# Kernel tuning notes

Hardware: AMD Instinct MI355X
Metric: run time of the kernel (lower is better)

The kernel has to match this reference:

```python
import jax, jax.numpy as jnp
import numpy as np

B, T, I, H, O = 128, 500, 512, 1024, 11
BETA, THRESH, GAMMA, SPARSITY = 0.9, 1.0, 0.5, 0.05

@jax.custom_vjp
def spike(x):
    return (x > 0).astype(x.dtype)

def _spike_fwd(x):
    return (x > 0).astype(x.dtype), x

def _spike_bwd(x, g):
    # surrogate gradient: gamma / (1 + |x|)^2
    return (g * GAMMA / jnp.square(1.0 + jnp.abs(x)),)

spike.defvjp(_spike_fwd, _spike_bwd)


def setup_inputs() -> dict:
    key = jax.random.key(0)
    k0, k1, k2, k3, k4 = jax.random.split(key, 5)
    x = jax.random.normal(k0, (B, T, I), jnp.float32)
    # xavier-uniform-like init for W_in / W_out, orthogonal-ish (scaled normal) for W_rec
    lim_in = (6.0 / (I + H)) ** 0.5
    lim_out = (6.0 / (H + O)) ** 0.5
    W_in = jax.random.uniform(k1, (I, H), jnp.float32, -lim_in, lim_in)
    W_rec = jax.random.normal(k2, (H, H), jnp.float32) / jnp.sqrt(jnp.float32(H))
    W_out = jax.random.uniform(k3, (H, O), jnp.float32, -lim_out, lim_out)
    # fixed sparse connectivity mask: Bernoulli(sparsity), no self-connections
    mask = (jax.random.uniform(k4, (H, H)) < SPARSITY).astype(jnp.float32)
    mask = mask * (1.0 - jnp.eye(H, dtype=jnp.float32))
    W_rec = W_rec * mask  # reset_parameters() applies mask at init when mask is not learnable
    h_bias = jnp.zeros((H,), jnp.float32)
    b_out = jnp.zeros((O,), jnp.float32)
    return {"x": x, "W_in": W_in, "W_rec": W_rec, "W_out": W_out,
            "h_bias": h_bias, "b_out": b_out, "mask": mask}


def reference(x, W_in, W_rec, W_out, h_bias, b_out, mask):
    W_eff = W_rec * mask                                   # masked recurrent weights [H,H]
    drive = jnp.einsum('bti,ih->bth', x, W_in) + h_bias    # per-step input drive [B,T,H]
    drive_t = jnp.swapaxes(drive, 0, 1)                    # [T,B,H]

    def step(carry, d_t):
        v, s = carry
        v = BETA * v + d_t + s @ W_eff                     # LIF membrane update
        s_new = spike(v - THRESH)                          # surrogate threshold spike
        v = v - jax.lax.stop_gradient(s_new) * THRESH      # subtract reset (detached)
        out_t = s_new @ W_out + b_out                      # per-step readout [B,O]
        return (v, s_new), out_t

    init = (jnp.zeros((x.shape[0], W_eff.shape[0]), x.dtype),
            jnp.zeros((x.shape[0], W_eff.shape[0]), x.dtype))
    _, outs = jax.lax.scan(step, init, drive_t)            # outs: [T,B,O]
    return jnp.mean(outs, axis=0)                          # 'rate' readout -> [B,O]
```

## Files before the change

kernel.cpp:

```cpp
#include <hip/hip_runtime.h>
#include <cstdint>
#include <cstddef>

#define B_ 128
#define T_ 500
#define I_ 512
#define H_ 1024
#define O_ 11
#define BETA 0.9f
#define THRESH 1.0f
#define K2_ 1536

typedef __attribute__((ext_vector_type(4))) float f32x4;
typedef __attribute__((ext_vector_type(8))) short bf16x8;
typedef __attribute__((ext_vector_type(4))) unsigned int u32x4;

__device__ __forceinline__ unsigned short bf16_rne(float f) {
  unsigned int u = __float_as_uint(f);
  unsigned int r = u + 0x7FFFu + ((u >> 16) & 1u);
  return (unsigned short)(r >> 16);
}
__device__ __forceinline__ float bf16_to_f(unsigned short h) {
  return __uint_as_float(((unsigned int)h) << 16);
}

__global__ void k_csr(const float* __restrict__ W_rec, const float* __restrict__ mask,
                      unsigned int* __restrict__ csr, unsigned int* __restrict__ rowhi) {
  int r = blockIdx.x * 4 + (threadIdx.x >> 6);
  int lane = threadIdx.x & 63;
  unsigned cnt = 0;
  const float* mrow = mask + (size_t)r * H_;
  const float* wrow = W_rec + (size_t)r * H_;
  for (int c = 0; c < 16; ++c) {
    float m = mrow[c * 64 + lane];
    bool nz = (m != 0.f);
    unsigned long long bb = __ballot(nz);
    unsigned pos = cnt + (unsigned)__popcll(bb & ((1ull << lane) - 1ull));
    if (nz) {
      float w = wrow[c * 64 + lane] * m;
      int wi = __float2int_rn(w * 8388608.f);
      wi = wi > 2097151 ? 2097151 : (wi < -2097151 ? -2097151 : wi);
      if (pos < 128u) csr[((size_t)r << 7) + pos] = (((unsigned)wi) << 10) | (unsigned)(c * 64 + lane);
    }
    cnt += (unsigned)__popcll(bb);
  }
  for (unsigned p = (cnt > 128u ? 128u : cnt) + (unsigned)lane; p < 128u; p += 64u)
    csr[((size_t)r << 7) + p] = (p & 63u);
  if (lane == 0) rowhi[r] = (cnt > 64u) ? 1u : 0u;
}

__global__ void k_build_wt(const float* __restrict__ W_in, unsigned short* __restrict__ Wt) {
  int n = blockIdx.y;
  int k2 = blockIdx.x * 256 + threadIdx.x;
  int i = k2 & 511;
  int c = k2 >> 9;
  float w = W_in[i * H_ + n];
  unsigned short hi = bf16_rne(w);
  unsigned short v = (c == 2) ? bf16_rne(w - bf16_to_f(hi)) : hi;
  Wt[(size_t)n * K2_ + k2] = v;
}

#define LDA 72
__global__ __launch_bounds__(512, 1) void k_gemm(const float* __restrict__ x,
                                                 const unsigned short* __restrict__ Wt,
                                                 float* __restrict__ drive,
                                                 int t0, int Tc) {
  __shared__ __align__(16) unsigned short As[128 * LDA];
  __shared__ __align__(16) unsigned short Bs[256 * LDA];
  int id = blockIdx.x;
  int mt = (id >> 5) * 8 + (id & 7);
  int nt = (id >> 3) & 3;
  if (mt >= Tc) return;
  int tid = threadIdx.x;
  int lane = tid & 63, w = tid >> 6;
  int wr = w >> 2, wc = w & 3;
  f32x4 acc[4][4] = {};
  int arow = tid >> 2, aq = tid & 3;
  int brow = tid >> 1, bh = tid & 1;
  int rr = mt * 128 + arow;
  int bb = rr / Tc, tt = rr - bb * Tc;
  const float* xrow = x + ((size_t)(bb * T_ + t0 + tt)) * I_ + aq * 16;
  const unsigned short* wtrow = Wt + (size_t)(nt * 256 + brow) * K2_ + bh * 32;
  for (int kt = 0; kt < K2_ / 64; ++kt) {
    int creg = kt >> 3;
    int i0 = (kt & 7) * 64;
    const float* ap = xrow + i0;
    float4 a0 = *(const float4*)(ap);
    float4 a1 = *(const float4*)(ap + 4);
    float4 a2 = *(const float4*)(ap + 8);
    float4 a3 = *(const float4*)(ap + 12);
    u32x4 b0 = *(const u32x4*)(wtrow + kt * 64);
    u32x4 b1 = *(const u32x4*)(wtrow + kt * 64 + 8);
    u32x4 b2 = *(const u32x4*)(wtrow + kt * 64 + 16);
    u32x4 b3 = *(const u32x4*)(wtrow + kt * 64 + 24);
    alignas(16) unsigned short o[16];
    float vv[16] = {a0.x, a0.y, a0.z, a0.w, a1.x, a1.y, a1.z, a1.w,
                    a2.x, a2.y, a2.z, a2.w, a3.x, a3.y, a3.z, a3.w};
#pragma unroll
    for (int j = 0; j < 16; ++j) {
      unsigned short hi = bf16_rne(vv[j]);
      o[j] = (creg == 1) ? bf16_rne(vv[j] - bf16_to_f(hi)) : hi;
    }
    __syncthreads();
    *(u32x4*)&As[arow * LDA + aq * 16] = *(u32x4*)o;
    *(u32x4*)&As[arow * LDA + aq * 16 + 8] = *(u32x4*)(o + 8);
    *(u32x4*)&Bs[brow * LDA + bh * 32] = b0;
    *(u32x4*)&Bs[brow * LDA + bh * 32 + 8] = b1;
    *(u32x4*)&Bs[brow * LDA + bh * 32 + 16] = b2;
    *(u32x4*)&Bs[brow * LDA + bh * 32 + 24] = b3;
    __syncthreads();
#pragma unroll
    for (int kk = 0; kk < 2; ++kk) {
      bf16x8 af[4], bf[4];
#pragma unroll
      for (int mi = 0; mi < 4; ++mi)
        af[mi] = *(const bf16x8*)&As[(wr * 64 + mi * 16 + (lane & 15)) * LDA + kk * 32 + (lane >> 4) * 8];
#pragma unroll
      for (int ni = 0; ni < 4; ++ni)
        bf[ni] = *(const bf16x8*)&Bs[(wc * 64 + ni * 16 + (lane & 15)) * LDA + kk * 32 + (lane >> 4) * 8];
#pragma unroll
      for (int mi = 0; mi < 4; ++mi)
#pragma unroll
        for (int ni = 0; ni < 4; ++ni)
          acc[mi][ni] = __builtin_amdgcn_mfma_f32_16x16x32_bf16(af[mi], bf[ni], acc[mi][ni], 0, 0, 0);
    }
  }
  int r0 = (lane >> 4) * 4, c0 = lane & 15;
#pragma unroll
  for (int mi = 0; mi < 4; ++mi) {
    int rowb = mt * 128 + wr * 64 + mi * 16 + r0;
#pragma unroll
    for (int ni = 0; ni < 4; ++ni) {
      int col = nt * 256 + wc * 64 + ni * 16 + c0;
#pragma unroll
      for (int r = 0; r < 4; ++r)
        drive[(size_t)(rowb + r) * H_ + col] = acc[mi][ni][r];
    }
  }
}

__device__ __forceinline__ void step_one(
    float dcur, int cur, int tid, int lane, unsigned wvu, unsigned myhi, float bias,
    const unsigned int* __restrict__ csr, int* accL, unsigned int* listL, unsigned int* fcL,
    float& v, float& s, float& cnt) {
  unsigned F = (unsigned)__builtin_amdgcn_readfirstlane((int)fcL[cur]);
  unsigned lo = (F * wvu) >> 4;
  unsigned hi = (F * (wvu + 1u)) >> 4;
  for (unsigned i0 = lo; i0 < hi; i0 += 8u) {
    unsigned idx = i0 + ((unsigned)lane & 7u);
    unsigned packed = listL[idx < hi ? idx : (hi - 1u)];
#define EDECL(n) unsigned e##n = (i0 + n##u < hi) ? (unsigned)__builtin_amdgcn_readlane((int)packed, n) : 1024u; \
                 unsigned ea##n = 0u, eb##n = 0u;
    EDECL(0) EDECL(1) EDECL(2) EDECL(3) EDECL(4) EDECL(5) EDECL(6) EDECL(7)
#undef EDECL
#define ELOAD(n) if (e##n != 1024u) { \
      const unsigned int* rp = csr + ((size_t)(e##n & 1023u) << 7); \
      ea##n = rp[lane]; \
      if (e##n & 4096u) eb##n = rp[64 + lane]; }
    ELOAD(0) ELOAD(1) ELOAD(2) ELOAD(3) ELOAD(4) ELOAD(5) ELOAD(6) ELOAD(7)
#undef ELOAD
#define EATOM(n) if (e##n != 1024u) { \
      atomicAdd(&accL[ea##n & 1023u], ((int)ea##n) >> 10); \
      if (e##n & 4096u) atomicAdd(&accL[eb##n & 1023u], ((int)eb##n) >> 10); }
    EATOM(0) EATOM(1) EATOM(2) EATOM(3) EATOM(4) EATOM(5) EATOM(6) EATOM(7)
#undef EATOM
  }
  __syncthreads();
  int ri = accL[tid];
  accL[tid] = 0;
  v = BETA * v + (dcur + bias) + (float)ri * 1.1920929e-7f;
  bool f = v > THRESH;
  v -= f ? THRESH : 0.f;
  cnt += f ? 1.f : 0.f;
  s = f ? 1.f : 0.f;
  unsigned long long bb = __ballot(f);
  unsigned n = (unsigned)__popcll(bb);
  unsigned pos = (unsigned)__popcll(bb & ((1ull << lane) - 1ull));
  unsigned wb = 0;
  if (lane == 0) wb = atomicAdd(&fcL[cur ^ 1], n);
  wb = (unsigned)__builtin_amdgcn_readfirstlane((int)wb);
  if (f) listL[wb + pos] = (unsigned)tid | myhi;
  if (tid == 0) fcL[cur] = 0;
  __syncthreads();
}

__global__ __launch_bounds__(1024, 1) void k_rsnn(
    const float* __restrict__ drive, const unsigned int* __restrict__ csr,
    const unsigned int* __restrict__ rowhi,
    const float* __restrict__ h_bias, const float* __restrict__ W_out,
    const float* __restrict__ b_out,
    float* __restrict__ state_v, float* __restrict__ state_s, float* __restrict__ state_c,
    float* __restrict__ out, int t0, int Tc, int last) {
  __shared__ int accL[H_];
  __shared__ unsigned int listL[H_];
  __shared__ unsigned int fcL[2];
  __shared__ float red[H_];
  __shared__ float part[352];
  int tid = threadIdx.x;
  int b = blockIdx.x;
  int lane = tid & 63;
  unsigned wvu = (unsigned)__builtin_amdgcn_readfirstlane(tid >> 6);
  float bias = h_bias[tid];
  unsigned myhi = rowhi[tid] << 12;
  float v, s, cnt;
  if (t0 == 0) { v = 0.f; s = 0.f; cnt = 0.f; }
  else { v = state_v[b * H_ + tid]; s = state_s[b * H_ + tid]; cnt = state_c[b * H_ + tid]; }
  accL[tid] = 0;
  if (tid < 2) fcL[tid] = 0;
  __syncthreads();
  {
    bool f0 = s > 0.f;
    unsigned long long bb = __ballot(f0);
    unsigned n = (unsigned)__popcll(bb);
    unsigned pos = (unsigned)__popcll(bb & ((1ull << lane) - 1ull));
    unsigned wb = 0;
    if (lane == 0) wb = atomicAdd(&fcL[0], n);
    wb = (unsigned)__builtin_amdgcn_readfirstlane((int)wb);
    if (f0) listL[wb + pos] = (unsigned)tid | myhi;
  }
  __syncthreads();
  const float* dptr = drive + (size_t)b * Tc * H_ + tid;
  for (int t8 = 0; t8 < Tc; t8 += 8) {
    float dd0 = (t8 + 0 < Tc) ? dptr[(size_t)(t8 + 0) * H_] : 0.f;
    float dd1 = (t8 + 1 < Tc) ? dptr[(size_t)(t8 + 1) * H_] : 0.f;
    float dd2 = (t8 + 2 < Tc) ? dptr[(size_t)(t8 + 2) * H_] : 0.f;
    float dd3 = (t8 + 3 < Tc) ? dptr[(size_t)(t8 + 3) * H_] : 0.f;
    float dd4 = (t8 + 4 < Tc) ? dptr[(size_t)(t8 + 4) * H_] : 0.f;
    float dd5 = (t8 + 5 < Tc) ? dptr[(size_t)(t8 + 5) * H_] : 0.f;
    float dd6 = (t8 + 6 < Tc) ? dptr[(size_t)(t8 + 6) * H_] : 0.f;
    float dd7 = (t8 + 7 < Tc) ? dptr[(size_t)(t8 + 7) * H_] : 0.f;
#define STEP(s_) if (t8 + s_ < Tc) \
    step_one(dd##s_, (s_ & 1), tid, lane, wvu, myhi, bias, csr, accL, listL, fcL, v, s, cnt);
    STEP(0) STEP(1) STEP(2) STEP(3) STEP(4) STEP(5) STEP(6) STEP(7)
#undef STEP
  }
  if (!last) {
    state_v[b * H_ + tid] = v; state_s[b * H_ + tid] = s; state_c[b * H_ + tid] = cnt;
  } else {
    red[tid] = cnt;
    __syncthreads();
    if (tid < 352) {
      int o = tid >> 5, seg = tid & 31;
      float p = 0.f;
      for (int j = 0; j < 32; ++j) {
        int hh = seg * 32 + j;
        p += red[hh] * W_out[hh * O_ + o];
      }
      part[tid] = p;
    }
    __syncthreads();
    if (tid < O_) {
      float sum = 0.f;
      for (int g = 0; g < 32; ++g) sum += part[(tid << 5) + g];
      out[b * O_ + tid] = b_out[tid] + sum * (1.0f / (float)T_);
    }
  }
}

extern "C" void kernel_launch(void* const* d_in, const int* in_sizes, int n_in,
                              void* d_out, int out_size, void* d_ws, size_t ws_size,
                              hipStream_t stream) {
  (void)in_sizes; (void)n_in; (void)out_size;
  const float* x = (const float*)d_in[0];
  const float* W_in = (const float*)d_in[1];
  const float* W_rec = (const float*)d_in[2];
  const float* W_out = (const float*)d_in[3];
  const float* h_bias = (const float*)d_in[4];
  const float* b_out = (const float*)d_in[5];
  const float* mask = (const float*)d_in[6];
  float* out = (float*)d_out;

  char* ws = (char*)d_ws;
  size_t off = 0;
  auto alloc = [&](size_t bytes) {
    void* p = ws + off;
    off = (off + bytes + 255) & ~(size_t)255;
    return p;
  };
  unsigned short* Wt = (unsigned short*)alloc((size_t)H_ * K2_ * 2);
  unsigned int* csr = (unsigned int*)alloc((size_t)H_ * 128 * 4);
  unsigned int* rowhi = (unsigned int*)alloc((size_t)H_ * 4);
  float* st_v = (float*)alloc((size_t)B_ * H_ * 4);
  float* st_s = (float*)alloc((size_t)B_ * H_ * 4);
  float* st_c = (float*)alloc((size_t)B_ * H_ * 4);
  size_t fixed = off;

  size_t per_t = (size_t)128 * 1024 * 4;
  int Tc = 1;
  if (ws_size > fixed + per_t) Tc = (int)((ws_size - fixed) / per_t);
  if (Tc > T_) Tc = T_;
  if (Tc < 1) Tc = 1;
  float* drive = (float*)alloc((size_t)128 * Tc * 1024 * 4);

  k_csr<<<dim3(256), dim3(256), 0, stream>>>(W_rec, mask, csr, rowhi);
  k_build_wt<<<dim3(6, 1024), dim3(256), 0, stream>>>(W_in, Wt);

  for (int t0 = 0; t0 < T_; t0 += Tc) {
    int tc = (Tc < T_ - t0) ? Tc : (T_ - t0);
    int groups = (tc + 7) / 8;
    k_gemm<<<dim3(groups * 32), dim3(512), 0, stream>>>(x, Wt, drive, t0, tc);
    k_rsnn<<<dim3(128), dim3(1024), 0, stream>>>(drive, csr, rowhi, h_bias, W_out, b_out,
                                                 st_v, st_s, st_c, out, t0, tc,
                                                 (t0 + tc >= T_) ? 1 : 0);
  }
}
```

Measured before the change: 999.0 us.

## Overlap input-drive GEMM with recurrent scan via fused kernel and double buffering

Splits the time axis into chunks of up to 128 steps with two drive buffers, and launches a fused kernel where the first 128 blocks run the recurrent spiking scan on chunk c while the remaining blocks compute the input-projection GEMM for chunk c+1. The GEMM body is reworked to use 1024 threads per block with an 8-wide warp grid, so both roles share one block size and a union of shared-memory layouts. This is meant to hide GEMM time behind the latency-bound scan, which leaves most CUs idle. In exchange it uses smaller chunks, so there are more launches and state save/restore round trips than when the whole sequence fits in workspace, and GEMM blocks compete with scan blocks for CUs.

```diff
diff --git a/kernel.cpp b/kernel.cpp
--- a/kernel.cpp
+++ b/kernel.cpp
@@ -10,10 +10,24 @@
 #define BETA 0.9f
 #define THRESH 1.0f
 #define K2_ 1536
+#define LDA 72
 
 typedef __attribute__((ext_vector_type(4))) float f32x4;
 typedef __attribute__((ext_vector_type(8))) short bf16x8;
 typedef __attribute__((ext_vector_type(4))) unsigned int u32x4;
+
+struct ScanSmem {
+  int accL[H_];
+  unsigned int listL[H_];
+  unsigned int fcL[2];
+  float red[H_];
+  float part[352];
+};
+struct GemmSmem {
+  alignas(16) unsigned short As[128 * LDA];
+  alignas(16) unsigned short Bs[256 * LDA];
+};
+union FusedSmem { ScanSmem s; GemmSmem g; };
 
 __device__ __forceinline__ unsigned short bf16_rne(float f) {
   unsigned int u = __float_as_uint(f);
@@ -60,68 +74,55 @@
   Wt[(size_t)n * K2_ + k2] = v;
 }
 
-#define LDA 72
-__global__ __launch_bounds__(512, 1) void k_gemm(const float* __restrict__ x,
-                                                 const unsigned short* __restrict__ Wt,
-                                                 float* __restrict__ drive,
-                                                 int t0, int Tc) {
-  __shared__ __align__(16) unsigned short As[128 * LDA];
-  __shared__ __align__(16) unsigned short Bs[256 * LDA];
-  int id = blockIdx.x;
+__device__ __forceinline__ void gemm_body(const float* __restrict__ x,
+                                          const unsigned short* __restrict__ Wt,
+                                          float* __restrict__ drive, int t0, int Tc,
+                                          int id, int tid,
+                                          unsigned short* As, unsigned short* Bs) {
   int mt = (id >> 5) * 8 + (id & 7);
   int nt = (id >> 3) & 3;
   if (mt >= Tc) return;
-  int tid = threadIdx.x;
   int lane = tid & 63, w = tid >> 6;
-  int wr = w >> 2, wc = w & 3;
-  f32x4 acc[4][4] = {};
-  int arow = tid >> 2, aq = tid & 3;
-  int brow = tid >> 1, bh = tid & 1;
+  int wr = w >> 3, wc = w & 7;
+  f32x4 acc[4][2] = {};
+  int arow = tid >> 3, aoct = tid & 7;
+  int brow = tid >> 2, bq = tid & 3;
   int rr = mt * 128 + arow;
   int bb = rr / Tc, tt = rr - bb * Tc;
-  const float* xrow = x + ((size_t)(bb * T_ + t0 + tt)) * I_ + aq * 16;
-  const unsigned short* wtrow = Wt + (size_t)(nt * 256 + brow) * K2_ + bh * 32;
+  const float* xrow = x + ((size_t)(bb * T_ + t0 + tt)) * I_ + aoct * 8;
+  const unsigned short* wtrow = Wt + (size_t)(nt * 256 + brow) * K2_ + bq * 16;
   for (int kt = 0; kt < K2_ / 64; ++kt) {
     int creg = kt >> 3;
-    int i0 = (kt & 7) * 64;
-    const float* ap = xrow + i0;
+    const float* ap = xrow + (kt & 7) * 64;
     float4 a0 = *(const float4*)(ap);
     float4 a1 = *(const float4*)(ap + 4);
-    float4 a2 = *(const float4*)(ap + 8);
-    float4 a3 = *(const float4*)(ap + 12);
     u32x4 b0 = *(const u32x4*)(wtrow + kt * 64);
     u32x4 b1 = *(const u32x4*)(wtrow + kt * 64 + 8);
-    u32x4 b2 = *(const u32x4*)(wtrow + kt * 64 + 16);
-    u32x4 b3 = *(const u32x4*)(wtrow + kt * 64 + 24);
-    alignas(16) unsigned short o[16];
-    float vv[16] = {a0.x, a0.y, a0.z, a0.w, a1.x, a1.y, a1.z, a1.w,
-                    a2.x, a2.y, a2.z, a2.w, a3.x, a3.y, a3.z, a3.w};
-#pragma unroll
-    for (int j = 0; j < 16; ++j) {
+    alignas(16) unsigned short o[8];
+    float vv[8] = {a0.x, a0.y, a0.z, a0.w, a1.x, a1.y, a1.z, a1.w};
+#pragma unroll
+    for (int j = 0; j < 8; ++j) {
       unsigned short hi = bf16_rne(vv[j]);
       o[j] = (creg == 1) ? bf16_rne(vv[j] - bf16_to_f(hi)) : hi;
     }
     __syncthreads();
-    *(u32x4*)&As[arow * LDA + aq * 16] = *(u32x4*)o;
-    *(u32x4*)&As[arow * LDA + aq * 16 + 8] = *(u32x4*)(o + 8);
-    *(u32x4*)&Bs[brow * LDA + bh * 32] = b0;
-    *(u32x4*)&Bs[brow * LDA + bh * 32 + 8] = b1;
-    *(u32x4*)&Bs[brow * LDA + bh * 32 + 16] = b2;
-    *(u32x4*)&Bs[brow * LDA + bh * 32 + 24] = b3;
+    *(u32x4*)&As[arow * LDA + aoct * 8] = *(u32x4*)o;
+    *(u32x4*)&Bs[brow * LDA + bq * 16] = b0;
+    *(u32x4*)&Bs[brow * LDA + bq * 16 + 8] = b1;
     __syncthreads();
 #pragma unroll
     for (int kk = 0; kk < 2; ++kk) {
-      bf16x8 af[4], bf[4];
+      bf16x8 af[4], bf[2];
 #pragma unroll
       for (int mi = 0; mi < 4; ++mi)
         af[mi] = *(const bf16x8*)&As[(wr * 64 + mi * 16 + (lane & 15)) * LDA + kk * 32 + (lane >> 4) * 8];
 #pragma unroll
-      for (int ni = 0; ni < 4; ++ni)
-        bf[ni] = *(const bf16x8*)&Bs[(wc * 64 + ni * 16 + (lane & 15)) * LDA + kk * 32 + (lane >> 4) * 8];
+      for (int ni = 0; ni < 2; ++ni)
+        bf[ni] = *(const bf16x8*)&Bs[(wc * 32 + ni * 16 + (lane & 15)) * LDA + kk * 32 + (lane >> 4) * 8];
 #pragma unroll
       for (int mi = 0; mi < 4; ++mi)
 #pragma unroll
-        for (int ni = 0; ni < 4; ++ni)
+        for (int ni = 0; ni < 2; ++ni)
           acc[mi][ni] = __builtin_amdgcn_mfma_f32_16x16x32_bf16(af[mi], bf[ni], acc[mi][ni], 0, 0, 0);
     }
   }
@@ -130,13 +131,20 @@
   for (int mi = 0; mi < 4; ++mi) {
     int rowb = mt * 128 + wr * 64 + mi * 16 + r0;
 #pragma unroll
-    for (int ni = 0; ni < 4; ++ni) {
-      int col = nt * 256 + wc * 64 + ni * 16 + c0;
+    for (int ni = 0; ni < 2; ++ni) {
+      int col = nt * 256 + wc * 32 + ni * 16 + c0;
 #pragma unroll
       for (int r = 0; r < 4; ++r)
         drive[(size_t)(rowb + r) * H_ + col] = acc[mi][ni][r];
     }
   }
+}
+
+__global__ __launch_bounds__(1024, 1) void k_gemm(const float* __restrict__ x,
+                                                  const unsigned short* __restrict__ Wt,
+                                                  float* __restrict__ drive, int t0, int Tc) {
+  __shared__ GemmSmem g;
+  gemm_body(x, Wt, drive, t0, Tc, blockIdx.x, threadIdx.x, g.As, g.Bs);
 }
 
 __device__ __forceinline__ void step_one(
@@ -184,20 +192,13 @@
   __syncthreads();
 }
 
-__global__ __launch_bounds__(1024, 1) void k_rsnn(
+__device__ __forceinline__ void scan_body(
     const float* __restrict__ drive, const unsigned int* __restrict__ csr,
     const unsigned int* __restrict__ rowhi,
     const float* __restrict__ h_bias, const float* __restrict__ W_out,
     const float* __restrict__ b_out,
     float* __restrict__ state_v, float* __restrict__ state_s, float* __restrict__ state_c,
-    float* __restrict__ out, int t0, int Tc, int last) {
-  __shared__ int accL[H_];
-  __shared__ unsigned int listL[H_];
-  __shared__ unsigned int fcL[2];
-  __shared__ float red[H_];
-  __shared__ float part[352];
-  int tid = threadIdx.x;
-  int b = blockIdx.x;
+    float* __restrict__ out, int t0, int Tc, int last, int b, int tid, ScanSmem& sm) {
   int lane = tid & 63;
   unsigned wvu = (unsigned)__builtin_amdgcn_readfirstlane(tid >> 6);
   float bias = h_bias[tid];
@@ -205,8 +206,8 @@
   float v, s, cnt;
   if (t0 == 0) { v = 0.f; s = 0.f; cnt = 0.f; }
   else { v = state_v[b * H_ + tid]; s = state_s[b * H_ + tid]; cnt = state_c[b * H_ + tid]; }
-  accL[tid] = 0;
-  if (tid < 2) fcL[tid] = 0;
+  sm.accL[tid] = 0;
+  if (tid < 2) sm.fcL[tid] = 0;
   __syncthreads();
   {
     bool f0 = s > 0.f;
@@ -214,9 +215,9 @@
     unsigned n = (unsigned)__popcll(bb);
     unsigned pos = (unsigned)__popcll(bb & ((1ull << lane) - 1ull));
     unsigned wb = 0;
-    if (lane == 0) wb = atomicAdd(&fcL[0], n);
+    if (lane == 0) wb = atomicAdd(&sm.fcL[0], n);
     wb = (unsigned)__builtin_amdgcn_readfirstlane((int)wb);
-    if (f0) listL[wb + pos] = (unsigned)tid | myhi;
+    if (f0) sm.listL[wb + pos] = (unsigned)tid | myhi;
   }
   __syncthreads();
   const float* dptr = drive + (size_t)b * Tc * H_ + tid;
@@ -230,30 +231,60 @@
     float dd6 = (t8 + 6 < Tc) ? dptr[(size_t)(t8 + 6) * H_] : 0.f;
     float dd7 = (t8 + 7 < Tc) ? dptr[(size_t)(t8 + 7) * H_] : 0.f;
 #define STEP(s_) if (t8 + s_ < Tc) \
-    step_one(dd##s_, (s_ & 1), tid, lane, wvu, myhi, bias, csr, accL, listL, fcL, v, s, cnt);
+    step_one(dd##s_, (s_ & 1), tid, lane, wvu, myhi, bias, csr, sm.accL, sm.listL, sm.fcL, v, s, cnt);
     STEP(0) STEP(1) STEP(2) STEP(3) STEP(4) STEP(5) STEP(6) STEP(7)
 #undef STEP
   }
   if (!last) {
     state_v[b * H_ + tid] = v; state_s[b * H_ + tid] = s; state_c[b * H_ + tid] = cnt;
   } else {
-    red[tid] = cnt;
+    sm.red[tid] = cnt;
     __syncthreads();
     if (tid < 352) {
       int o = tid >> 5, seg = tid & 31;
       float p = 0.f;
       for (int j = 0; j < 32; ++j) {
         int hh = seg * 32 + j;
-        p += red[hh] * W_out[hh * O_ + o];
+        p += sm.red[hh] * W_out[hh * O_ + o];
       }
-      part[tid] = p;
+      sm.part[tid] = p;
     }
     __syncthreads();
     if (tid < O_) {
       float sum = 0.f;
-      for (int g = 0; g < 32; ++g) sum += part[(tid << 5) + g];
+      for (int g = 0; g < 32; ++g) sum += sm.part[(tid << 5) + g];
       out[b * O_ + tid] = b_out[tid] + sum * (1.0f / (float)T_);
     }
+  }
+}
+
+__global__ __launch_bounds__(1024, 1) void k_rsnn(
+    const float* __restrict__ drive, const unsigned int* __restrict__ csr,
+    const unsigned int* __restrict__ rowhi,
+    const float* __restrict__ h_bias, const float* __restrict__ W_out,
+    const float* __restrict__ b_out,
+    float* __restrict__ state_v, float* __restrict__ state_s, float* __restrict__ state_c,
+    float* __restrict__ out, int t0, int Tc, int last) {
+  __shared__ ScanSmem sm;
+  scan_body(drive, csr, rowhi, h_bias, W_out, b_out, state_v, state_s, state_c, out,
+            t0, Tc, last, blockIdx.x, threadIdx.x, sm);
+}
+
+__global__ __launch_bounds__(1024, 1) void k_fused(
+    const float* __restrict__ drive_s, const unsigned int* __restrict__ csr,
+    const unsigned int* __restrict__ rowhi,
+    const float* __restrict__ h_bias, const float* __restrict__ W_out,
+    const float* __restrict__ b_out,
+    float* __restrict__ state_v, float* __restrict__ state_s, float* __restrict__ state_c,
+    float* __restrict__ out, int t0s, int Tcs,
+    const float* __restrict__ x, const unsigned short* __restrict__ Wt,
+    float* __restrict__ drive_g, int t0g, int Tcg) {
+  __shared__ FusedSmem sm;
+  if (blockIdx.x < 128) {
+    scan_body(drive_s, csr, rowhi, h_bias, W_out, b_out, state_v, state_s, state_c, out,
+              t0s, Tcs, 0, blockIdx.x, threadIdx.x, sm.s);
+  } else {
+    gemm_body(x, Wt, drive_g, t0g, Tcg, blockIdx.x - 128, threadIdx.x, sm.g.As, sm.g.Bs);
   }
 }
 
@@ -285,22 +316,36 @@
   float* st_c = (float*)alloc((size_t)B_ * H_ * 4);
   size_t fixed = off;
 
-  size_t per_t = (size_t)128 * 1024 * 4;
-  int Tc = 1;
-  if (ws_size > fixed + per_t) Tc = (int)((ws_size - fixed) / per_t);
-  if (Tc > T_) Tc = T_;
-  if (Tc < 1) Tc = 1;
-  float* drive = (float*)alloc((size_t)128 * Tc * 1024 * 4);
+  size_t avail = ws_size > fixed ? ws_size - fixed : 0;
+  const size_t per_t = (size_t)128 * 1024 * 4;
+  int TC = 128;
+  while (TC > 1 && 2u * (size_t)TC * per_t > avail) TC >>= 1;
+  float* driveA = (float*)alloc((size_t)TC * per_t);
+  float* driveB = (float*)alloc((size_t)TC * per_t);
+  int C = (T_ + TC - 1) / TC;
 
   k_csr<<<dim3(256), dim3(256), 0, stream>>>(W_rec, mask, csr, rowhi);
   k_build_wt<<<dim3(6, 1024), dim3(256), 0, stream>>>(W_in, Wt);
 
-  for (int t0 = 0; t0 < T_; t0 += Tc) {
-    int tc = (Tc < T_ - t0) ? Tc : (T_ - t0);
-    int groups = (tc + 7) / 8;
-    k_gemm<<<dim3(groups * 32), dim3(512), 0, stream>>>(x, Wt, drive, t0, tc);
-    k_rsnn<<<dim3(128), dim3(1024), 0, stream>>>(drive, csr, rowhi, h_bias, W_out, b_out,
-                                                 st_v, st_s, st_c, out, t0, tc,
-                                                 (t0 + tc >= T_) ? 1 : 0);
-  }
-}
+  {
+    int tc0 = T_ < TC ? T_ : TC;
+    k_gemm<<<dim3(((tc0 + 7) / 8) * 32), dim3(1024), 0, stream>>>(x, Wt, driveA, 0, tc0);
+  }
+  for (int c = 0; c < C; ++c) {
+    int t0 = c * TC;
+    int tc = (T_ - t0) < TC ? (T_ - t0) : TC;
+    float* bufS = (c & 1) ? driveB : driveA;
+    if (c + 1 < C) {
+      int t0n = (c + 1) * TC;
+      int tcn = (T_ - t0n) < TC ? (T_ - t0n) : TC;
+      float* bufG = ((c + 1) & 1) ? driveB : driveA;
+      int gblocks = ((tcn + 7) / 8) * 32;
+      k_fused<<<dim3(128 + gblocks), dim3(1024), 0, stream>>>(
+          bufS, csr, rowhi, h_bias, W_out, b_out, st_v, st_s, st_c, out, t0, tc,
+          x, Wt, bufG, t0n, tcn);
+    } else {
+      k_rsnn<<<dim3(128), dim3(1024), 0, stream>>>(bufS, csr, rowhi, h_bias, W_out, b_out,
+                                                   st_v, st_s, st_c, out, t0, tc, 1);
+    }
+  }
+}
```

Result: faster. 862.5 us (-13.7%).
